# Kernel tuning notes

Hardware: AMD Instinct MI355X
Metric: run time of the kernel (lower is better)

Reference implementation:

```python
import jax, jax.numpy as jnp
import numpy as np

NUM_NODES = 4904
EMBED_DIM = 300
NUM_CLASSES = 14


def setup_inputs() -> dict:
    key = jax.random.key(0)
    k1, k2, k3, k4, k5, k6, k7, k8 = jax.random.split(key, 8)
    B, L, K = 128, 512, 8
    master_nodes = jax.random.randint(k1, (B, L), 0, NUM_NODES + 1)
    slave_nodes = jax.random.randint(k2, (B, L, K), 0, NUM_NODES + 1)
    slave_edges = jax.random.randint(k3, (B, L, K), 0, NUM_NODES * NUM_NODES + 1)
    # Embedding tables (padding_idx=0 -> zero row)
    R = jax.random.normal(k4, (NUM_NODES + 1, EMBED_DIM), dtype=jnp.float32)
    R = R.at[0].set(0.0)
    E = jax.random.normal(k5, (NUM_NODES * NUM_NODES + 1, 1), dtype=jnp.float32)
    E = E.at[0].set(0.0)
    N = jax.random.normal(k6, (NUM_NODES + 1, 1), dtype=jnp.float32)
    N = N.at[0].set(0.0)
    # fc: Linear(300 -> 14)
    bound = 1.0 / np.sqrt(EMBED_DIM)
    W = jax.random.uniform(k7, (NUM_CLASSES, EMBED_DIM), minval=-bound, maxval=bound, dtype=jnp.float32)
    b = jax.random.uniform(k8, (NUM_CLASSES,), minval=-bound, maxval=bound, dtype=jnp.float32)
    return {"master_nodes": master_nodes, "slave_nodes": slave_nodes,
            "slave_edges": slave_edges, "R": R, "E": E, "N": N, "W": W, "b": b}


def reference(master_nodes, slave_nodes, slave_edges, R, E, N, W, b):
    Rn = R[master_nodes]          # [B, L, D]
    Ra = R[slave_nodes]           # [B, L, K, D]
    Ean = E[slave_edges]          # [B, L, K, 1]
    Mn = jnp.max(Ra * Ean, axis=2)  # [B, L, D] max-pool over neighbors
    Nn = N[master_nodes]          # [B, L, 1] gate
    x = (1.0 - Nn) * Mn + Nn * Rn  # [B, L, D]
    x = jnp.sum(x, axis=1)         # [B, D]
    h = jax.nn.relu(x @ W.T + b)   # [B, C]
    # Dropout is identity in eval mode; softmax over classes (dim=1)
    return jax.nn.softmax(h, axis=1)
```

## Files before the change

kernel.cpp:

```cpp
#include <hip/hip_runtime.h>
#include <hip/hip_fp16.h>
#include <math.h>

#define BB 128
#define LL 512
#define KK 8
#define DD 300
#define D2 150
#define CC 14
#define L_PER_BLOCK 8
#define UNROLL 4
#define NUM_LC (LL / L_PER_BLOCK)

#define R_F4_ELEMS ((4905 * 300) / 4)

typedef _Float16 h2 __attribute__((ext_vector_type(2)));
typedef float    f4 __attribute__((ext_vector_type(4)));

__global__ __launch_bounds__(256) void prep(
    const f4* __restrict__ R4, h2* __restrict__ R16)
{
    const int i = blockIdx.x * 256 + threadIdx.x;
    if (i < R_F4_ELEMS) {
        const f4 f = __builtin_nontemporal_load(R4 + i);
        h2 a; a.x = (_Float16)f.x; a.y = (_Float16)f.y;
        h2 b; b.x = (_Float16)f.z; b.y = (_Float16)f.w;
        R16[2 * i]     = a;
        R16[2 * i + 1] = b;
    }
}

__global__ __launch_bounds__(192) void gnn_agg(
    const int* __restrict__ master, const int* __restrict__ slaves,
    const int* __restrict__ edges, const float* __restrict__ E,
    const float* __restrict__ N, const h2* __restrict__ Rv,
    float2* __restrict__ Xp2)
{
    const int b  = blockIdx.x;
    const int lc = blockIdx.y;
    const int t  = threadIdx.x;
    const bool act = (t < D2);
    const int bl_base = b * LL + lc * L_PER_BLOCK;

    __shared__ __align__(16) int ebuf[L_PER_BLOCK * KK];
    __shared__ float nnbuf[L_PER_BLOCK];

    if (t < L_PER_BLOCK * KK) {
        const int eidx = edges[bl_base * KK + t];
        const _Float16 ev = (_Float16)__builtin_nontemporal_load(E + eidx);
        h2 p; p.x = ev; p.y = ev;
        ebuf[t] = __builtin_bit_cast(int, p);
    } else if (t < L_PER_BLOCK * KK + L_PER_BLOCK) {
        const int l = t - L_PER_BLOCK * KK;
        nnbuf[l] = N[master[bl_base + l]];
    }
    __syncthreads();

    float accx = 0.f, accy = 0.f;

    for (int lg = 0; lg < L_PER_BLOCK; lg += UNROLL) {
        int   offm[UNROLL], offs[UNROLL][KK];
        int4  ea[UNROLL], eb2[UNROLL];
        float nn[UNROLL];

#pragma unroll
        for (int u = 0; u < UNROLL; ++u) {
            const int bl = bl_base + lg + u;
            offm[u] = master[bl] * D2;
#pragma unroll
            for (int k = 0; k < KK; ++k)
                offs[u][k] = slaves[bl * KK + k] * D2;
            ea[u]  = *(const int4*)&ebuf[(lg + u) * KK];
            eb2[u] = *(const int4*)&ebuf[(lg + u) * KK + 4];
            nn[u]  = nnbuf[lg + u];
        }

        if (act) {
            h2 r[UNROLL][KK], rm[UNROLL];
#pragma unroll
            for (int u = 0; u < UNROLL; ++u) {
#pragma unroll
                for (int k = 0; k < KK; ++k) r[u][k] = (Rv + offs[u][k])[t];
            }
#pragma unroll
            for (int u = 0; u < UNROLL; ++u) rm[u] = (Rv + offm[u])[t];

#pragma unroll
            for (int u = 0; u < UNROLL; ++u) {
                const int ev[KK] = { ea[u].x, ea[u].y, ea[u].z, ea[u].w,
                                     eb2[u].x, eb2[u].y, eb2[u].z, eb2[u].w };
                h2 mx = r[u][0] * __builtin_bit_cast(h2, ev[0]);
#pragma unroll
                for (int k = 1; k < KK; ++k)
                    mx = __builtin_elementwise_max(
                        mx, r[u][k] * __builtin_bit_cast(h2, ev[k]));
                const float n = nn[u], a = 1.f - n;
                accx = fmaf(a, (float)mx.x, fmaf(n, (float)rm[u].x, accx));
                accy = fmaf(a, (float)mx.y, fmaf(n, (float)rm[u].y, accy));
            }
        }
    }
    if (act) {
        const float2 v = make_float2(accx, accy);
        __builtin_nontemporal_store(
            __builtin_bit_cast(unsigned long long, v),
            (unsigned long long*)(Xp2 + (lc * BB + b) * D2 + t));
    }
}

__global__ __launch_bounds__(320) void fc_softmax(
    const float2* __restrict__ Xp2, const float* __restrict__ W,
    const float* __restrict__ bias, float* __restrict__ out)
{
    const int b = blockIdx.x;
    const int t = threadIdx.x;
    __shared__ float sx[DD];
    __shared__ float h[CC];

    if (t < D2) {
        float ax = 0.f, ay = 0.f;
        const float2* p = Xp2 + b * D2 + t;
#pragma unroll 8
        for (int lc = 0; lc < NUM_LC; ++lc) {
            const float2 v = p[(long)lc * BB * D2];
            ax += v.x; ay += v.y;
        }
        sx[2 * t]     = ax;
        sx[2 * t + 1] = ay;
    }
    __syncthreads();

    const int c = t >> 4;
    const int j = t & 15;
    if (c < CC) {
        float acc = 0.f;
        const float* w = W + c * DD;
        for (int d = j; d < DD; d += 16) acc += sx[d] * w[d];
#pragma unroll
        for (int off = 8; off > 0; off >>= 1) acc += __shfl_down(acc, off, 16);
        if (j == 0) h[c] = fmaxf(acc + bias[c], 0.f);
    }
    __syncthreads();
    if (t < CC) {
        float mx = -INFINITY;
#pragma unroll
        for (int i = 0; i < CC; ++i) mx = fmaxf(mx, h[i]);
        float s = 0.f;
#pragma unroll
        for (int i = 0; i < CC; ++i) s += expf(h[i] - mx);
        out[b * CC + t] = expf(h[t] - mx) / s;
    }
}

extern "C" void kernel_launch(void* const* d_in, const int* in_sizes, int n_in,
                              void* d_out, int out_size, void* d_ws, size_t ws_size,
                              hipStream_t stream) {
    const int*   master = (const int*)d_in[0];
    const int*   slaves = (const int*)d_in[1];
    const int*   edges  = (const int*)d_in[2];
    const float* R      = (const float*)d_in[3];
    const float* E      = (const float*)d_in[4];
    const float* N      = (const float*)d_in[5];
    const float* W      = (const float*)d_in[6];
    const float* bias   = (const float*)d_in[7];
    float* out = (float*)d_out;

    char* ws = (char*)d_ws;
    h2*     R16 = (h2*)ws;
    float2* Xp2 = (float2*)(ws + 2943104);

    prep<<<(R_F4_ELEMS + 255) / 256, 256, 0, stream>>>((const f4*)R, R16);

    dim3 grid(BB, NUM_LC);
    gnn_agg<<<grid, 192, 0, stream>>>(master, slaves, edges, E, N, R16, Xp2);

    fc_softmax<<<BB, 320, 0, stream>>>(Xp2, W, bias, out);
}
```

Baseline: 184.5 us.

## Widen gather to fp16x4 and split block into four L-streams with smem reduction

Each thread now gathers 8-byte fp16x4 chunks of R, so 75 threads cover a row. The block holds four such streams, each handling 8 L positions, 32 L per block in total. Stream partials are reduced in shared memory, which cuts the partial-sum buffer and the fc_softmax reduction by 4x. Slave and master offsets are preloaded into shared memory once per block rather than read from global memory by every thread. This trades fewer, larger gather requests and fewer blocks against an extra sync and shared-memory reduction; 20 of the 320 threads sit idle.

```diff
diff --git a/kernel.cpp b/kernel.cpp
--- a/kernel.cpp
+++ b/kernel.cpp
@@ -1,132 +1,150 @@
 #include <hip/hip_runtime.h>
-#include <hip/hip_fp16.h>
 #include <math.h>
 
 #define BB 128
 #define LL 512
 #define KK 8
 #define DD 300
-#define D2 150
+#define D4 75
 #define CC 14
-#define L_PER_BLOCK 8
-#define UNROLL 4
+#define STREAMS 4
+#define L_PER_STREAM 8
+#define L_PER_BLOCK 32
+#define UNROLL 2
 #define NUM_LC (LL / L_PER_BLOCK)
 
 #define R_F4_ELEMS ((4905 * 300) / 4)
 
 typedef _Float16 h2 __attribute__((ext_vector_type(2)));
+typedef _Float16 h4 __attribute__((ext_vector_type(4)));
 typedef float    f4 __attribute__((ext_vector_type(4)));
 
 __global__ __launch_bounds__(256) void prep(
-    const f4* __restrict__ R4, h2* __restrict__ R16)
+    const f4* __restrict__ R4, h4* __restrict__ R16)
 {
     const int i = blockIdx.x * 256 + threadIdx.x;
     if (i < R_F4_ELEMS) {
         const f4 f = __builtin_nontemporal_load(R4 + i);
-        h2 a; a.x = (_Float16)f.x; a.y = (_Float16)f.y;
-        h2 b; b.x = (_Float16)f.z; b.y = (_Float16)f.w;
-        R16[2 * i]     = a;
-        R16[2 * i + 1] = b;
+        h4 o;
+        o.x = (_Float16)f.x; o.y = (_Float16)f.y;
+        o.z = (_Float16)f.z; o.w = (_Float16)f.w;
+        R16[i] = o;
     }
 }
 
-__global__ __launch_bounds__(192) void gnn_agg(
+__global__ __launch_bounds__(320, 4) void gnn_agg(
     const int* __restrict__ master, const int* __restrict__ slaves,
     const int* __restrict__ edges, const float* __restrict__ E,
-    const float* __restrict__ N, const h2* __restrict__ Rv,
-    float2* __restrict__ Xp2)
+    const float* __restrict__ N, const h4* __restrict__ Rv,
+    f4* __restrict__ Xp)
 {
     const int b  = blockIdx.x;
     const int lc = blockIdx.y;
     const int t  = threadIdx.x;
-    const bool act = (t < D2);
-    const int bl_base = b * LL + lc * L_PER_BLOCK;
+    const int bl0 = b * LL + lc * L_PER_BLOCK;
 
-    __shared__ __align__(16) int ebuf[L_PER_BLOCK * KK];
+    __shared__ int   olds[L_PER_BLOCK][9];
+    __shared__ int   ebuf[L_PER_BLOCK * KK];
     __shared__ float nnbuf[L_PER_BLOCK];
+    __shared__ f4    sred[STREAMS][D4];
 
     if (t < L_PER_BLOCK * KK) {
-        const int eidx = edges[bl_base * KK + t];
+        const int eidx = __builtin_nontemporal_load(edges + bl0 * KK + t);
         const _Float16 ev = (_Float16)__builtin_nontemporal_load(E + eidx);
         h2 p; p.x = ev; p.y = ev;
         ebuf[t] = __builtin_bit_cast(int, p);
+        const int sn = __builtin_nontemporal_load(slaves + bl0 * KK + t);
+        olds[t >> 3][t & 7] = sn * D4;
     } else if (t < L_PER_BLOCK * KK + L_PER_BLOCK) {
         const int l = t - L_PER_BLOCK * KK;
-        nnbuf[l] = N[master[bl_base + l]];
+        const int m = __builtin_nontemporal_load(master + bl0 + l);
+        olds[l][8] = m * D4;
+        nnbuf[l]   = N[m];
     }
     __syncthreads();
 
-    float accx = 0.f, accy = 0.f;
+    const bool act = (t < STREAMS * D4);
+    const int  s   = act ? t / D4 : 0;
+    const int  pos = t - s * D4;
 
-    for (int lg = 0; lg < L_PER_BLOCK; lg += UNROLL) {
-        int   offm[UNROLL], offs[UNROLL][KK];
-        int4  ea[UNROLL], eb2[UNROLL];
-        float nn[UNROLL];
+    if (act) {
+        const int ls0 = s * L_PER_STREAM;
+        float a0 = 0.f, a1 = 0.f, a2 = 0.f, a3 = 0.f;
 
+        for (int lg = 0; lg < L_PER_STREAM; lg += UNROLL) {
+            int   off[UNROLL][9], ev[UNROLL][KK];
+            float nn[UNROLL];
 #pragma unroll
-        for (int u = 0; u < UNROLL; ++u) {
-            const int bl = bl_base + lg + u;
-            offm[u] = master[bl] * D2;
+            for (int u = 0; u < UNROLL; ++u) {
+                const int l = ls0 + lg + u;
 #pragma unroll
-            for (int k = 0; k < KK; ++k)
-                offs[u][k] = slaves[bl * KK + k] * D2;
-            ea[u]  = *(const int4*)&ebuf[(lg + u) * KK];
-            eb2[u] = *(const int4*)&ebuf[(lg + u) * KK + 4];
-            nn[u]  = nnbuf[lg + u];
-        }
+                for (int k = 0; k < 9; ++k)  off[u][k] = olds[l][k];
+#pragma unroll
+                for (int k = 0; k < KK; ++k) ev[u][k]  = ebuf[l * KK + k];
+                nn[u] = nnbuf[l];
+            }
 
-        if (act) {
-            h2 r[UNROLL][KK], rm[UNROLL];
+            h4 r[UNROLL][KK], rm[UNROLL];
 #pragma unroll
             for (int u = 0; u < UNROLL; ++u) {
 #pragma unroll
-                for (int k = 0; k < KK; ++k) r[u][k] = (Rv + offs[u][k])[t];
+                for (int k = 0; k < KK; ++k)
+                    r[u][k] = Rv[off[u][k] + pos];
+                rm[u] = Rv[off[u][8] + pos];
             }
-#pragma unroll
-            for (int u = 0; u < UNROLL; ++u) rm[u] = (Rv + offm[u])[t];
 
 #pragma unroll
             for (int u = 0; u < UNROLL; ++u) {
-                const int ev[KK] = { ea[u].x, ea[u].y, ea[u].z, ea[u].w,
-                                     eb2[u].x, eb2[u].y, eb2[u].z, eb2[u].w };
-                h2 mx = r[u][0] * __builtin_bit_cast(h2, ev[0]);
+                h2 e0 = __builtin_bit_cast(h2, ev[u][0]);
+                h4 e4 = {e0.x, e0.y, e0.x, e0.y};
+                h4 mx = r[u][0] * e4;
 #pragma unroll
-                for (int k = 1; k < KK; ++k)
-                    mx = __builtin_elementwise_max(
-                        mx, r[u][k] * __builtin_bit_cast(h2, ev[k]));
-                const float n = nn[u], a = 1.f - n;
-                accx = fmaf(a, (float)mx.x, fmaf(n, (float)rm[u].x, accx));
-                accy = fmaf(a, (float)mx.y, fmaf(n, (float)rm[u].y, accy));
+                for (int k = 1; k < KK; ++k) {
+                    h2 ek2 = __builtin_bit_cast(h2, ev[u][k]);
+                    h4 ek  = {ek2.x, ek2.y, ek2.x, ek2.y};
+                    mx = __builtin_elementwise_max(mx, r[u][k] * ek);
+                }
+                const float n = nn[u], g = 1.f - n;
+                a0 = fmaf(g, (float)mx.x, fmaf(n, (float)rm[u].x, a0));
+                a1 = fmaf(g, (float)mx.y, fmaf(n, (float)rm[u].y, a1));
+                a2 = fmaf(g, (float)mx.z, fmaf(n, (float)rm[u].z, a2));
+                a3 = fmaf(g, (float)mx.w, fmaf(n, (float)rm[u].w, a3));
             }
         }
+        f4 v; v.x = a0; v.y = a1; v.z = a2; v.w = a3;
+        sred[s][pos] = v;
     }
-    if (act) {
-        const float2 v = make_float2(accx, accy);
-        __builtin_nontemporal_store(
-            __builtin_bit_cast(unsigned long long, v),
-            (unsigned long long*)(Xp2 + (lc * BB + b) * D2 + t));
+    __syncthreads();
+
+    if (t < D4) {
+        const f4 v0 = sred[0][t], v1 = sred[1][t], v2 = sred[2][t], v3 = sred[3][t];
+        f4 v;
+        v.x = (v0.x + v1.x) + (v2.x + v3.x);
+        v.y = (v0.y + v1.y) + (v2.y + v3.y);
+        v.z = (v0.z + v1.z) + (v2.z + v3.z);
+        v.w = (v0.w + v1.w) + (v2.w + v3.w);
+        __builtin_nontemporal_store(v, Xp + (lc * BB + b) * D4 + t);
     }
 }
 
 __global__ __launch_bounds__(320) void fc_softmax(
-    const float2* __restrict__ Xp2, const float* __restrict__ W,
+    const f4* __restrict__ Xp, const float* __restrict__ W,
     const float* __restrict__ bias, float* __restrict__ out)
 {
     const int b = blockIdx.x;
     const int t = threadIdx.x;
-    __shared__ float sx[DD];
+    __shared__ __align__(16) float sx[DD];
     __shared__ float h[CC];
 
-    if (t < D2) {
-        float ax = 0.f, ay = 0.f;
-        const float2* p = Xp2 + b * D2 + t;
-#pragma unroll 8
+    if (t < D4) {
+        f4 a = {0.f, 0.f, 0.f, 0.f};
+        const f4* p = Xp + b * D4 + t;
+#pragma unroll
         for (int lc = 0; lc < NUM_LC; ++lc) {
-            const float2 v = p[(long)lc * BB * D2];
-            ax += v.x; ay += v.y;
+            const f4 v = __builtin_nontemporal_load(p + lc * (BB * D4));
+            a.x += v.x; a.y += v.y; a.z += v.z; a.w += v.w;
         }
-        sx[2 * t]     = ax;
-        sx[2 * t + 1] = ay;
+        ((f4*)sx)[t] = a;
     }
     __syncthreads();
 
@@ -145,10 +163,10 @@
         float mx = -INFINITY;
 #pragma unroll
         for (int i = 0; i < CC; ++i) mx = fmaxf(mx, h[i]);
-        float s = 0.f;
+        float ssum = 0.f;
 #pragma unroll
-        for (int i = 0; i < CC; ++i) s += expf(h[i] - mx);
-        out[b * CC + t] = expf(h[t] - mx) / s;
+        for (int i = 0; i < CC; ++i) ssum += expf(h[i] - mx);
+        out[b * CC + t] = expf(h[t] - mx) / ssum;
     }
 }
 
@@ -165,14 +183,14 @@
     const float* bias   = (const float*)d_in[7];
     float* out = (float*)d_out;
 
-    char* ws = (char*)d_ws;
-    h2*     R16 = (h2*)ws;
-    float2* Xp2 = (float2*)(ws + 2943104);
+    char* ws  = (char*)d_ws;
+    h4*   R16 = (h4*)ws;
+    f4*   Xp  = (f4*)(ws + 2943104);
 
     prep<<<(R_F4_ELEMS + 255) / 256, 256, 0, stream>>>((const f4*)R, R16);
 
     dim3 grid(BB, NUM_LC);
-    gnn_agg<<<grid, 192, 0, stream>>>(master, slaves, edges, E, N, R16, Xp2);
+    gnn_agg<<<grid, STREAMS * 80, 0, stream>>>(master, slaves, edges, E, N, R16, Xp);
 
-    fc_softmax<<<BB, 320, 0, stream>>>(Xp2, W, bias, out);
+    fc_softmax<<<BB, 320, 0, stream>>>(Xp, W, bias, out);
 }
```

Measured after the change: 184.8 us. Within noise of the previous version (+0.2%).
